# Performance work log

Measured on AMD Instinct MI355X. Metric: run time of the kernel, lower is better.

The kernel has to match this reference:

```python
import jax, jax.numpy as jnp
import numpy as np

NUM_BLOCKS = 8
D_MODEL = 256
FLAT_DIM = NUM_BLOCKS * NUM_BLOCKS + NUM_BLOCKS * 4  # 96


def setup_inputs() -> dict:
    key = jax.random.key(0)
    k1, k2, k3, k4, k5 = jax.random.split(key, 5)
    B, S, Blk = 8, 16384, NUM_BLOCKS
    bit_tensor = jax.random.randint(k1, (B, S, Blk, 8), 0, 2, dtype=jnp.int32)
    macro_stimulus = jax.random.uniform(k2, (B, S), dtype=jnp.float32)
    # torch.rand(...) * 0.1 equivalent (diag masking done in reference, as in torch)
    W_init = jax.random.uniform(k3, (B, S, Blk, Blk), dtype=jnp.float32) * 0.1
    lin_w = jax.random.normal(k4, (D_MODEL, FLAT_DIM), dtype=jnp.float32) / np.sqrt(FLAT_DIM)
    lin_b = jax.random.normal(k5, (D_MODEL,), dtype=jnp.float32) * 0.01
    return {
        "bit_tensor": bit_tensor,
        "macro_stimulus": macro_stimulus,
        "W_init": W_init,
        "lin_w": lin_w,
        "lin_b": lin_b,
        "internal_steps": 10,
    }


def _decode_bits_to_epgl(bit_tensor):
    # [B,S,Blk,8] int bits -> [B,S,Blk,4] floats in {0, 1/3, 2/3, 1}
    b = bit_tensor.astype(jnp.float32)
    return (b[..., 0::2] * 2.0 + b[..., 1::2]) / 3.0  # pairs (0,1),(2,3),(4,5),(6,7) -> E,P,G,L


def _safe_pdist(h):
    # pairwise L2 over last dim: h [B,S,Blk,4] -> [B,S,Blk,Blk]; sqrt-safe at 0 (diagonal)
    diff = h[..., :, None, :] - h[..., None, :, :]
    d2 = jnp.sum(diff * diff, axis=-1)
    return jnp.where(d2 > 0, jnp.sqrt(jnp.where(d2 > 0, d2, 1.0)), 0.0)


def _step(h, W, stim, eye):
    clamp = lambda x: jnp.clip(x, 0.0, 1.0)
    E, P, G, L = h[..., 0], h[..., 1], h[..., 2], h[..., 3]
    W_ns = W * (1.0 - eye)
    inflow = jnp.matmul(W_ns, h)                         # [B,S,Blk,4]
    total_w = jnp.sum(W_ns, axis=-1, keepdims=True) + 1e-8
    neigh = inflow / total_w
    En, Pn, Gn, Ln = neigh[..., 0], neigh[..., 1], neigh[..., 2], neigh[..., 3]
    E_new = clamp(E + 0.3 * stim - 0.4 * P - 0.2 * G)
    P_new = clamp(P + 0.5 * stim + 0.3 * (Pn - P) - 0.2 * E)
    G_new = clamp(G + 0.4 * E * (1.0 - P) + 0.2 * (Gn - G) - 0.3 * P)
    good_neighbor = 0.5 * En + 0.5 * Gn
    L_new = clamp(L + 0.4 * good_neighbor + 0.3 * (Ln - L) - 0.3 * P)
    h_new = jnp.stack([E_new, P_new, G_new, L_new], axis=-1)
    h_diff = _safe_pdist(h_new)                          # cdist(h_new, h_new, p=2)
    mutual_L = (L_new[..., :, None] + L_new[..., None, :]) * 0.5
    W_new = clamp(W + 0.1 * mutual_L * h_diff - 0.05 * W) * (1.0 - eye)
    return h_new, W_new


def _forward(bit_tensor, macro_stimulus, W_init, lin_w, lin_b, internal_steps):
    B, S, Blk, _ = bit_tensor.shape
    eye = jnp.eye(Blk, dtype=jnp.float32)
    h = _decode_bits_to_epgl(bit_tensor)                 # [B,S,Blk,4]
    W = W_init * (1.0 - eye)                             # [B,S,Blk,Blk]
    stim = jnp.broadcast_to(macro_stimulus[..., None], (B, S, Blk))

    def body(carry, _):
        h, W = carry
        h, W = _step(h, W, stim, eye)
        return (h, W), None

    (h, W), _ = jax.lax.scan(body, (h, W), None, length=internal_steps)
    phys = jnp.concatenate([h.reshape(B, S, -1), W.reshape(B, S, -1)], axis=-1)  # [B,S,96]
    macro_embedding = jnp.einsum('bsf,df->bsd', phys, lin_w) + lin_b
    return macro_embedding, h, W


def reference(bit_tensor, macro_stimulus, W_init, lin_w, lin_b, internal_steps):
    return _forward(bit_tensor, macro_stimulus, W_init, lin_w, lin_b, internal_steps)
```

## Files before the change

### kernel.cpp

```cpp
#include <hip/hip_runtime.h>

#define NB 8
#define DM 256
#define FD 96
#define SLD 104

using half8 = _Float16 __attribute__((ext_vector_type(8)));
using half4 = _Float16 __attribute__((ext_vector_type(4)));
using f32x4 = float __attribute__((ext_vector_type(4)));
using f2    = float __attribute__((ext_vector_type(2)));

__device__ __forceinline__ float clamp01(float x) { return fminf(fmaxf(x, 0.0f), 1.0f); }

__global__ void bprep_kernel(const float* __restrict__ lin_w,
                             _Float16* __restrict__ Bpre)
{
    const int fb = blockIdx.x * 256 + threadIdx.x;
    const int ks = fb >> 10, nbv = (fb >> 6) & 15, ll = fb & 63;
    const float* lwrow = lin_w + (size_t)(nbv * 16 + (ll & 15)) * FD
                               + (ks * 32 + 4 * (ll >> 4));
    float4 lo = *reinterpret_cast<const float4*>(lwrow);
    float4 hi = *reinterpret_cast<const float4*>(lwrow + 16);
    half8 v;
    v[0] = (_Float16)lo.x; v[1] = (_Float16)lo.y; v[2] = (_Float16)lo.z; v[3] = (_Float16)lo.w;
    v[4] = (_Float16)hi.x; v[5] = (_Float16)hi.y; v[6] = (_Float16)hi.z; v[7] = (_Float16)hi.w;
    *reinterpret_cast<half8*>(Bpre + (size_t)fb * 8) = v;
}

__global__ __launch_bounds__(256, 2) void fused_kernel(
    const int* __restrict__ bits,
    const float* __restrict__ stim_in,
    const float* __restrict__ Winit,
    const int* __restrict__ steps_ptr,
    const _Float16* __restrict__ Bpre,
    const float* __restrict__ lin_b,
    float* __restrict__ out_emb,
    float* __restrict__ out_h,
    float* __restrict__ out_W)
{
    __shared__ __align__(16) char smem[64 * 132 * 4];
    _Float16* S    = reinterpret_cast<_Float16*>(smem);
    float*    Cbuf = reinterpret_cast<float*>(smem);

    const int tid  = threadIdx.x;
    const int pos0 = blockIdx.x * 128;
    const int p    = tid >> 1;
    const int pos  = pos0 + p;
    const int sub  = tid & 1;
    const int steps = steps_ptr[0];

    f2 hA[8];
    f2 hB[8];
    f2 W2[4][4];

    const int4* bp = reinterpret_cast<const int4*>(bits + (size_t)pos * 64 + sub * 32);
    #pragma unroll
    for (int b = 0; b < 4; ++b) {
        int4 lo = bp[2 * b + 0];
        int4 hi = bp[2 * b + 1];
        hA[b].x = (float)(lo.x * 2 + lo.y) / 3.0f;
        hA[b].y = (float)(lo.z * 2 + lo.w) / 3.0f;
        hB[b].x = (float)(hi.x * 2 + hi.y) / 3.0f;
        hB[b].y = (float)(hi.z * 2 + hi.w) / 3.0f;
    }
    #pragma unroll
    for (int b = 0; b < 4; ++b) {
        hA[4 + b].x = __shfl_xor(hA[b].x, 1, 64);
        hA[4 + b].y = __shfl_xor(hA[b].y, 1, 64);
        hB[4 + b].x = __shfl_xor(hB[b].x, 1, 64);
        hB[4 + b].y = __shfl_xor(hB[b].y, 1, 64);
    }

    const int co_own = sub * 4;
    const int co_oth = 4 - sub * 4;
    #pragma unroll
    for (int i = 0; i < 4; ++i) {
        const float* rowp = Winit + (size_t)pos * 64 + (size_t)(co_own + i) * 8;
        float4 a = *reinterpret_cast<const float4*>(rowp + co_own);
        float4 b = *reinterpret_cast<const float4*>(rowp + co_oth);
        W2[i][0] = (f2){a.x, a.y};
        W2[i][1] = (f2){a.z, a.w};
        W2[i][2] = (f2){b.x, b.y};
        W2[i][3] = (f2){b.z, b.w};
        if (i & 1) W2[i][i >> 1].y = 0.0f; else W2[i][i >> 1].x = 0.0f;
    }

    const float stim = stim_in[pos];

    for (int st = 0; st < steps; ++st) {
        f2 nbA[4], nbB[4];
        #pragma unroll
        for (int i = 0; i < 4; ++i) {
            f2 sA = {0.f, 0.f}, sB = {0.f, 0.f};
            #pragma unroll
            for (int jc = 0; jc < 4; ++jc) {
                f2 wv = W2[i][jc];
                f2 w0 = {wv.x, wv.x};
                f2 w1 = {wv.y, wv.y};
                sA = __builtin_elementwise_fma(w0, hA[2 * jc],     sA);
                sA = __builtin_elementwise_fma(w1, hA[2 * jc + 1], sA);
                sB = __builtin_elementwise_fma(w0, hB[2 * jc],     sB);
                sB = __builtin_elementwise_fma(w1, hB[2 * jc + 1], sB);
            }
            float tw = W2[i][0].x; tw += W2[i][0].y;
            tw += W2[i][1].x;      tw += W2[i][1].y;
            tw += W2[i][2].x;      tw += W2[i][2].y;
            tw += W2[i][3].x;      tw += W2[i][3].y;
            float inv = __builtin_amdgcn_rcpf(tw + 1e-8f);
            f2 inv2 = {inv, inv};
            nbA[i] = sA * inv2;
            nbB[i] = sB * inv2;
        }
        #pragma unroll
        for (int i = 0; i < 4; ++i) {
            float E = hA[i].x, P = hA[i].y, G = hB[i].x, L = hB[i].y;
            float En = nbA[i].x, Pn = nbA[i].y, Gn = nbB[i].x, Ln = nbB[i].y;
            float E_new = clamp01(E + 0.3f * stim - 0.4f * P - 0.2f * G);
            float P_new = clamp01(P + 0.5f * stim + 0.3f * (Pn - P) - 0.2f * E);
            float G_new = clamp01(G + 0.4f * E * (1.0f - P) + 0.2f * (Gn - G) - 0.3f * P);
            float good  = 0.5f * En + 0.5f * Gn;
            float L_new = clamp01(L + 0.4f * good + 0.3f * (Ln - L) - 0.3f * P);
            hA[i] = (f2){E_new, P_new};
            hB[i] = (f2){G_new, L_new};
        }
        #pragma unroll
        for (int b = 0; b < 4; ++b) {
            hA[4 + b].x = __shfl_xor(hA[b].x, 1, 64);
            hA[4 + b].y = __shfl_xor(hA[b].y, 1, 64);
            hB[4 + b].x = __shfl_xor(hB[b].x, 1, 64);
            hB[4 + b].y = __shfl_xor(hB[b].y, 1, 64);
        }
        #pragma unroll
        for (int i = 0; i < 4; ++i) {
            #pragma unroll
            for (int j = i + 1; j < 8; ++j) {
                float d0 = hA[i].x - hA[j].x;
                float d1 = hA[i].y - hA[j].y;
                float d2 = hB[i].x - hB[j].x;
                float d3 = hB[i].y - hB[j].y;
                float q = d0 * d0 + d1 * d1 + d2 * d2 + d3 * d3;
                float dist = __builtin_amdgcn_sqrtf(q);
                float inc = 0.1f * (0.5f * (hB[i].y + hB[j].y)) * dist;
                float wij = (j & 1) ? W2[i][j >> 1].y : W2[i][j >> 1].x;
                wij = clamp01(wij + inc - 0.05f * wij);
                if (j & 1) W2[i][j >> 1].y = wij; else W2[i][j >> 1].x = wij;
                if (j < 4) {
                    float wji = (i & 1) ? W2[j][i >> 1].y : W2[j][i >> 1].x;
                    wji = clamp01(wji + inc - 0.05f * wji);
                    if (i & 1) W2[j][i >> 1].y = wji; else W2[j][i >> 1].x = wji;
                }
            }
        }
    }

    {
        _Float16* sp = S + p * SLD;
        half8 v0, v1;
        v0[0] = (_Float16)hA[0].x; v0[1] = (_Float16)hA[0].y;
        v0[2] = (_Float16)hB[0].x; v0[3] = (_Float16)hB[0].y;
        v0[4] = (_Float16)hA[1].x; v0[5] = (_Float16)hA[1].y;
        v0[6] = (_Float16)hB[1].x; v0[7] = (_Float16)hB[1].y;
        v1[0] = (_Float16)hA[2].x; v1[1] = (_Float16)hA[2].y;
        v1[2] = (_Float16)hB[2].x; v1[3] = (_Float16)hB[2].y;
        v1[4] = (_Float16)hA[3].x; v1[5] = (_Float16)hA[3].y;
        v1[6] = (_Float16)hB[3].x; v1[7] = (_Float16)hB[3].y;
        *reinterpret_cast<half8*>(sp + sub * 16)     = v0;
        *reinterpret_cast<half8*>(sp + sub * 16 + 8) = v1;
        #pragma unroll
        for (int i = 0; i < 4; ++i) {
            half8 wv;
            #pragma unroll
            for (int gc = 0; gc < 8; ++gc) {
                const int lc0 = gc;
                const int lc1 = (gc + 4) & 7;
                float vs0 = (lc0 & 1) ? W2[i][lc0 >> 1].y : W2[i][lc0 >> 1].x;
                float vs1 = (lc1 & 1) ? W2[i][lc1 >> 1].y : W2[i][lc1 >> 1].x;
                wv[gc] = (_Float16)((sub == 0) ? vs0 : vs1);
            }
            *reinterpret_cast<half8*>(sp + 32 + (co_own + i) * 8) = wv;
        }
    }
    __syncthreads();

    #pragma unroll
    for (int i = 0; i < 4; ++i) {
        const int flat4 = i * 1024 + tid * 4;
        const int row = flat4 >> 5, feat = flat4 & 31;
        half4 v = *reinterpret_cast<const half4*>(S + row * SLD + feat);
        float4 o = make_float4((float)v[0], (float)v[1], (float)v[2], (float)v[3]);
        *reinterpret_cast<float4*>(out_h + (size_t)pos0 * 32 + flat4) = o;
    }
    #pragma unroll
    for (int i = 0; i < 8; ++i) {
        const int flat4 = i * 1024 + tid * 4;
        const int row = flat4 >> 6, feat = flat4 & 63;
        half4 v = *reinterpret_cast<const half4*>(S + row * SLD + 32 + feat);
        float4 o = make_float4((float)v[0], (float)v[1], (float)v[2], (float)v[3]);
        *reinterpret_cast<float4*>(out_W + (size_t)pos0 * 64 + flat4) = o;
    }

    const int w = tid >> 6, l = tid & 63;
    const int k0q = 4 * (l >> 4);
    half8 afr[2][3];
    #pragma unroll
    for (int t = 0; t < 2; ++t) {
        const int r = t * 64 + w * 16 + (l & 15);
        #pragma unroll
        for (int ks = 0; ks < 3; ++ks) {
            half4 lo = *reinterpret_cast<const half4*>(S + r * SLD + ks * 32 + k0q);
            half4 hi = *reinterpret_cast<const half4*>(S + r * SLD + ks * 32 + 16 + k0q);
            afr[t][ks] = __builtin_shufflevector(lo, hi, 0, 1, 2, 3, 4, 5, 6, 7);
        }
    }
    __syncthreads();

    #pragma unroll
    for (int t = 0; t < 2; ++t) {
        f32x4 acc[16];
        #pragma unroll
        for (int nbv = 0; nbv < 16; ++nbv) acc[nbv] = (f32x4){0.f, 0.f, 0.f, 0.f};
        #pragma unroll
        for (int ks = 0; ks < 3; ++ks) {
            #pragma unroll
            for (int nbv = 0; nbv < 16; ++nbv) {
                half8 b = *reinterpret_cast<const half8*>(Bpre + (size_t)((ks * 16 + nbv) * 64 + l) * 8);
                acc[nbv] = __builtin_amdgcn_mfma_f32_16x16x32_f16(afr[t][ks], b, acc[nbv], 0, 0, 0);
            }
        }
        #pragma unroll
        for (int c = 0; c < 2; ++c) {
            #pragma unroll
            for (int nn = 0; nn < 8; ++nn) {
                const int nbv = c * 8 + nn;
                #pragma unroll
                for (int r = 0; r < 4; ++r) {
                    const int row = w * 16 + 4 * (l >> 4) + r;
                    Cbuf[row * 132 + nn * 16 + (l & 15)] = acc[nbv][r];
                }
            }
            __syncthreads();
            const float4 biasv = reinterpret_cast<const float4*>(lin_b)[c * 32 + (l & 31)];
            #pragma unroll
            for (int rep = 0; rep < 8; ++rep) {
                const int row = w * 16 + rep * 2 + (l >> 5);
                float4 v = *reinterpret_cast<const float4*>(Cbuf + row * 132 + (l & 31) * 4);
                v.x += biasv.x; v.y += biasv.y; v.z += biasv.z; v.w += biasv.w;
                *reinterpret_cast<float4*>(out_emb + (size_t)(pos0 + t * 64 + row) * DM
                                           + c * 128 + (l & 31) * 4) = v;
            }
            __syncthreads();
        }
    }
}

extern "C" void kernel_launch(void* const* d_in, const int* in_sizes, int n_in,
                              void* d_out, int out_size, void* d_ws, size_t ws_size,
                              hipStream_t stream) {
    const int*   bits  = (const int*)d_in[0];
    const float* stim  = (const float*)d_in[1];
    const float* Winit = (const float*)d_in[2];
    const float* lin_w = (const float*)d_in[3];
    const float* lin_b = (const float*)d_in[4];
    const int*   steps = (const int*)d_in[5];

    const int npos = in_sizes[1];

    float* out_emb = (float*)d_out;
    float* out_h   = out_emb + (size_t)npos * DM;
    float* out_W   = out_h + (size_t)npos * 32;
    _Float16* Bpre = (_Float16*)d_ws;

    hipLaunchKernelGGL(bprep_kernel, dim3(12), dim3(256), 0, stream, lin_w, Bpre);
    hipLaunchKernelGGL(fused_kernel, dim3(npos / 128), dim3(256), 0, stream,
                       bits, stim, Winit, steps, Bpre, lin_b,
                       out_emb, out_h, out_W);
}
```

Baseline: 75.25 us.

## Assign one position per thread, drop shuffles, write MFMA output directly

Each thread now owns a whole 8-block position, so the two-thread split and its per-step cross-lane shuffles go away and W is held as a full 8x8 register tile. The symmetric W update is vectorised with packed two-wide math. The epilogue writes MFMA accumulators plus bias straight to global memory instead of staging them through LDS with extra barriers. In exchange register pressure roughly doubles (launch bounds relaxed to one block per SIMD hint), the grid halves to 256 positions per block, and the output stores become narrower and less coalesced.

```diff
diff --git a/kernel.cpp b/kernel.cpp
--- a/kernel.cpp
+++ b/kernel.cpp
@@ -11,6 +11,10 @@
 using f2    = float __attribute__((ext_vector_type(2)));
 
 __device__ __forceinline__ float clamp01(float x) { return fminf(fmaxf(x, 0.0f), 1.0f); }
+__device__ __forceinline__ f2 pkclamp01(f2 x) {
+    const f2 lo = {0.0f, 0.0f}, hi = {1.0f, 1.0f};
+    return __builtin_elementwise_min(__builtin_elementwise_max(x, lo), hi);
+}
 
 __global__ void bprep_kernel(const float* __restrict__ lin_w,
                              _Float16* __restrict__ Bpre)
@@ -27,7 +31,7 @@
     *reinterpret_cast<half8*>(Bpre + (size_t)fb * 8) = v;
 }
 
-__global__ __launch_bounds__(256, 2) void fused_kernel(
+__global__ __launch_bounds__(256, 1) void fused_kernel(
     const int* __restrict__ bits,
     const float* __restrict__ stim_in,
     const float* __restrict__ Winit,
@@ -38,24 +42,20 @@
     float* __restrict__ out_h,
     float* __restrict__ out_W)
 {
-    __shared__ __align__(16) char smem[64 * 132 * 4];
-    _Float16* S    = reinterpret_cast<_Float16*>(smem);
-    float*    Cbuf = reinterpret_cast<float*>(smem);
+    __shared__ __align__(16) _Float16 S[256 * SLD];
 
     const int tid  = threadIdx.x;
-    const int pos0 = blockIdx.x * 128;
-    const int p    = tid >> 1;
-    const int pos  = pos0 + p;
-    const int sub  = tid & 1;
+    const int pos0 = blockIdx.x * 256;
+    const int pos  = pos0 + tid;
     const int steps = steps_ptr[0];
 
     f2 hA[8];
     f2 hB[8];
-    f2 W2[4][4];
-
-    const int4* bp = reinterpret_cast<const int4*>(bits + (size_t)pos * 64 + sub * 32);
-    #pragma unroll
-    for (int b = 0; b < 4; ++b) {
+    f2 W2[8][4];
+
+    const int4* bp = reinterpret_cast<const int4*>(bits + (size_t)pos * 64);
+    #pragma unroll
+    for (int b = 0; b < 8; ++b) {
         int4 lo = bp[2 * b + 0];
         int4 hi = bp[2 * b + 1];
         hA[b].x = (float)(lo.x * 2 + lo.y) / 3.0f;
@@ -63,21 +63,12 @@
         hB[b].x = (float)(hi.x * 2 + hi.y) / 3.0f;
         hB[b].y = (float)(hi.z * 2 + hi.w) / 3.0f;
     }
-    #pragma unroll
-    for (int b = 0; b < 4; ++b) {
-        hA[4 + b].x = __shfl_xor(hA[b].x, 1, 64);
-        hA[4 + b].y = __shfl_xor(hA[b].y, 1, 64);
-        hB[4 + b].x = __shfl_xor(hB[b].x, 1, 64);
-        hB[4 + b].y = __shfl_xor(hB[b].y, 1, 64);
-    }
-
-    const int co_own = sub * 4;
-    const int co_oth = 4 - sub * 4;
-    #pragma unroll
-    for (int i = 0; i < 4; ++i) {
-        const float* rowp = Winit + (size_t)pos * 64 + (size_t)(co_own + i) * 8;
-        float4 a = *reinterpret_cast<const float4*>(rowp + co_own);
-        float4 b = *reinterpret_cast<const float4*>(rowp + co_oth);
+
+    const float4* wp = reinterpret_cast<const float4*>(Winit + (size_t)pos * 64);
+    #pragma unroll
+    for (int i = 0; i < 8; ++i) {
+        float4 a = wp[2 * i + 0];
+        float4 b = wp[2 * i + 1];
         W2[i][0] = (f2){a.x, a.y};
         W2[i][1] = (f2){a.z, a.w};
         W2[i][2] = (f2){b.x, b.y};
@@ -88,9 +79,9 @@
     const float stim = stim_in[pos];
 
     for (int st = 0; st < steps; ++st) {
-        f2 nbA[4], nbB[4];
-        #pragma unroll
-        for (int i = 0; i < 4; ++i) {
+        f2 nbA[8], nbB[8];
+        #pragma unroll
+        for (int i = 0; i < 8; ++i) {
             f2 sA = {0.f, 0.f}, sB = {0.f, 0.f};
             #pragma unroll
             for (int jc = 0; jc < 4; ++jc) {
@@ -112,7 +103,7 @@
             nbB[i] = sB * inv2;
         }
         #pragma unroll
-        for (int i = 0; i < 4; ++i) {
+        for (int i = 0; i < 8; ++i) {
             float E = hA[i].x, P = hA[i].y, G = hB[i].x, L = hB[i].y;
             float En = nbA[i].x, Pn = nbA[i].y, Gn = nbB[i].x, Ln = nbB[i].y;
             float E_new = clamp01(E + 0.3f * stim - 0.4f * P - 0.2f * G);
@@ -124,16 +115,9 @@
             hB[i] = (f2){G_new, L_new};
         }
         #pragma unroll
-        for (int b = 0; b < 4; ++b) {
-            hA[4 + b].x = __shfl_xor(hA[b].x, 1, 64);
-            hA[4 + b].y = __shfl_xor(hA[b].y, 1, 64);
-            hB[4 + b].x = __shfl_xor(hB[b].x, 1, 64);
-            hB[4 + b].y = __shfl_xor(hB[b].y, 1, 64);
-        }
-        #pragma unroll
-        for (int i = 0; i < 4; ++i) {
-            #pragma unroll
-            for (int j = i + 1; j < 8; ++j) {
+        for (int i = 0; i < 8; ++i) {
+            if ((i & 1) == 0) {
+                const int j = i + 1;
                 float d0 = hA[i].x - hA[j].x;
                 float d1 = hA[i].y - hA[j].y;
                 float d2 = hB[i].x - hB[j].x;
@@ -141,49 +125,63 @@
                 float q = d0 * d0 + d1 * d1 + d2 * d2 + d3 * d3;
                 float dist = __builtin_amdgcn_sqrtf(q);
                 float inc = 0.1f * (0.5f * (hB[i].y + hB[j].y)) * dist;
-                float wij = (j & 1) ? W2[i][j >> 1].y : W2[i][j >> 1].x;
-                wij = clamp01(wij + inc - 0.05f * wij);
-                if (j & 1) W2[i][j >> 1].y = wij; else W2[i][j >> 1].x = wij;
-                if (j < 4) {
-                    float wji = (i & 1) ? W2[j][i >> 1].y : W2[j][i >> 1].x;
-                    wji = clamp01(wji + inc - 0.05f * wji);
-                    if (i & 1) W2[j][i >> 1].y = wji; else W2[j][i >> 1].x = wji;
-                }
+                float wij = W2[i][i >> 1].y;
+                float wji = W2[j][i >> 1].x;
+                W2[i][i >> 1].y = clamp01(wij + inc - 0.05f * wij);
+                W2[j][i >> 1].x = clamp01(wji + inc - 0.05f * wji);
+            }
+            #pragma unroll
+            for (int c = 0; c < 4; ++c) {
+                if (c <= (i >> 1)) continue;
+                const int j1 = 2 * c, j2 = 2 * c + 1;
+                f2 iAx = {hA[i].x, hA[i].x}, iAy = {hA[i].y, hA[i].y};
+                f2 iBx = {hB[i].x, hB[i].x}, iBy = {hB[i].y, hB[i].y};
+                f2 d0v = iAx - (f2){hA[j1].x, hA[j2].x};
+                f2 d1v = iAy - (f2){hA[j1].y, hA[j2].y};
+                f2 d2v = iBx - (f2){hB[j1].x, hB[j2].x};
+                f2 d3v = iBy - (f2){hB[j1].y, hB[j2].y};
+                f2 qv = d0v * d0v + d1v * d1v + d2v * d2v + d3v * d3v;
+                f2 distv = {__builtin_amdgcn_sqrtf(qv.x), __builtin_amdgcn_sqrtf(qv.y)};
+                f2 Lsum  = iBy + (f2){hB[j1].y, hB[j2].y};
+                const f2 c01 = {0.1f, 0.1f}, ch = {0.5f, 0.5f}, c05 = {0.05f, 0.05f};
+                f2 incv = c01 * (ch * Lsum) * distv;
+                f2 Wv = W2[i][c];
+                W2[i][c] = pkclamp01(Wv + incv - c05 * Wv);
+                float wj1 = (i & 1) ? W2[j1][i >> 1].y : W2[j1][i >> 1].x;
+                float wj2 = (i & 1) ? W2[j2][i >> 1].y : W2[j2][i >> 1].x;
+                wj1 = clamp01(wj1 + incv.x - 0.05f * wj1);
+                wj2 = clamp01(wj2 + incv.y - 0.05f * wj2);
+                if (i & 1) { W2[j1][i >> 1].y = wj1; W2[j2][i >> 1].y = wj2; }
+                else       { W2[j1][i >> 1].x = wj1; W2[j2][i >> 1].x = wj2; }
             }
         }
     }
 
     {
-        _Float16* sp = S + p * SLD;
-        half8 v0, v1;
-        v0[0] = (_Float16)hA[0].x; v0[1] = (_Float16)hA[0].y;
-        v0[2] = (_Float16)hB[0].x; v0[3] = (_Float16)hB[0].y;
-        v0[4] = (_Float16)hA[1].x; v0[5] = (_Float16)hA[1].y;
-        v0[6] = (_Float16)hB[1].x; v0[7] = (_Float16)hB[1].y;
-        v1[0] = (_Float16)hA[2].x; v1[1] = (_Float16)hA[2].y;
-        v1[2] = (_Float16)hB[2].x; v1[3] = (_Float16)hB[2].y;
-        v1[4] = (_Float16)hA[3].x; v1[5] = (_Float16)hA[3].y;
-        v1[6] = (_Float16)hB[3].x; v1[7] = (_Float16)hB[3].y;
-        *reinterpret_cast<half8*>(sp + sub * 16)     = v0;
-        *reinterpret_cast<half8*>(sp + sub * 16 + 8) = v1;
-        #pragma unroll
-        for (int i = 0; i < 4; ++i) {
+        _Float16* sp = S + tid * SLD;
+        #pragma unroll
+        for (int b2 = 0; b2 < 4; ++b2) {
+            half8 v;
+            v[0] = (_Float16)hA[2 * b2].x;     v[1] = (_Float16)hA[2 * b2].y;
+            v[2] = (_Float16)hB[2 * b2].x;     v[3] = (_Float16)hB[2 * b2].y;
+            v[4] = (_Float16)hA[2 * b2 + 1].x; v[5] = (_Float16)hA[2 * b2 + 1].y;
+            v[6] = (_Float16)hB[2 * b2 + 1].x; v[7] = (_Float16)hB[2 * b2 + 1].y;
+            *reinterpret_cast<half8*>(sp + b2 * 8) = v;
+        }
+        #pragma unroll
+        for (int r = 0; r < 8; ++r) {
             half8 wv;
-            #pragma unroll
-            for (int gc = 0; gc < 8; ++gc) {
-                const int lc0 = gc;
-                const int lc1 = (gc + 4) & 7;
-                float vs0 = (lc0 & 1) ? W2[i][lc0 >> 1].y : W2[i][lc0 >> 1].x;
-                float vs1 = (lc1 & 1) ? W2[i][lc1 >> 1].y : W2[i][lc1 >> 1].x;
-                wv[gc] = (_Float16)((sub == 0) ? vs0 : vs1);
-            }
-            *reinterpret_cast<half8*>(sp + 32 + (co_own + i) * 8) = wv;
+            wv[0] = (_Float16)W2[r][0].x; wv[1] = (_Float16)W2[r][0].y;
+            wv[2] = (_Float16)W2[r][1].x; wv[3] = (_Float16)W2[r][1].y;
+            wv[4] = (_Float16)W2[r][2].x; wv[5] = (_Float16)W2[r][2].y;
+            wv[6] = (_Float16)W2[r][3].x; wv[7] = (_Float16)W2[r][3].y;
+            *reinterpret_cast<half8*>(sp + 32 + r * 8) = wv;
         }
     }
     __syncthreads();
 
     #pragma unroll
-    for (int i = 0; i < 4; ++i) {
+    for (int i = 0; i < 8; ++i) {
         const int flat4 = i * 1024 + tid * 4;
         const int row = flat4 >> 5, feat = flat4 & 31;
         half4 v = *reinterpret_cast<const half4*>(S + row * SLD + feat);
@@ -191,7 +189,7 @@
         *reinterpret_cast<float4*>(out_h + (size_t)pos0 * 32 + flat4) = o;
     }
     #pragma unroll
-    for (int i = 0; i < 8; ++i) {
+    for (int i = 0; i < 16; ++i) {
         const int flat4 = i * 1024 + tid * 4;
         const int row = flat4 >> 6, feat = flat4 & 63;
         half4 v = *reinterpret_cast<const half4*>(S + row * SLD + 32 + feat);
@@ -201,21 +199,21 @@
 
     const int w = tid >> 6, l = tid & 63;
     const int k0q = 4 * (l >> 4);
-    half8 afr[2][3];
-    #pragma unroll
-    for (int t = 0; t < 2; ++t) {
+    float blin[16];
+    #pragma unroll
+    for (int nbv = 0; nbv < 16; ++nbv)
+        blin[nbv] = lin_b[nbv * 16 + (l & 15)];
+
+    #pragma unroll
+    for (int t = 0; t < 4; ++t) {
         const int r = t * 64 + w * 16 + (l & 15);
+        half8 afr[3];
         #pragma unroll
         for (int ks = 0; ks < 3; ++ks) {
             half4 lo = *reinterpret_cast<const half4*>(S + r * SLD + ks * 32 + k0q);
             half4 hi = *reinterpret_cast<const half4*>(S + r * SLD + ks * 32 + 16 + k0q);
-            afr[t][ks] = __builtin_shufflevector(lo, hi, 0, 1, 2, 3, 4, 5, 6, 7);
-        }
-    }
-    __syncthreads();
-
-    #pragma unroll
-    for (int t = 0; t < 2; ++t) {
+            afr[ks] = __builtin_shufflevector(lo, hi, 0, 1, 2, 3, 4, 5, 6, 7);
+        }
         f32x4 acc[16];
         #pragma unroll
         for (int nbv = 0; nbv < 16; ++nbv) acc[nbv] = (f32x4){0.f, 0.f, 0.f, 0.f};
@@ -224,31 +222,15 @@
             #pragma unroll
             for (int nbv = 0; nbv < 16; ++nbv) {
                 half8 b = *reinterpret_cast<const half8*>(Bpre + (size_t)((ks * 16 + nbv) * 64 + l) * 8);
-                acc[nbv] = __builtin_amdgcn_mfma_f32_16x16x32_f16(afr[t][ks], b, acc[nbv], 0, 0, 0);
-            }
-        }
-        #pragma unroll
-        for (int c = 0; c < 2; ++c) {
-            #pragma unroll
-            for (int nn = 0; nn < 8; ++nn) {
-                const int nbv = c * 8 + nn;
-                #pragma unroll
-                for (int r = 0; r < 4; ++r) {
-                    const int row = w * 16 + 4 * (l >> 4) + r;
-                    Cbuf[row * 132 + nn * 16 + (l & 15)] = acc[nbv][r];
-                }
-            }
-            __syncthreads();
-            const float4 biasv = reinterpret_cast<const float4*>(lin_b)[c * 32 + (l & 31)];
-            #pragma unroll
-            for (int rep = 0; rep < 8; ++rep) {
-                const int row = w * 16 + rep * 2 + (l >> 5);
-                float4 v = *reinterpret_cast<const float4*>(Cbuf + row * 132 + (l & 31) * 4);
-                v.x += biasv.x; v.y += biasv.y; v.z += biasv.z; v.w += biasv.w;
-                *reinterpret_cast<float4*>(out_emb + (size_t)(pos0 + t * 64 + row) * DM
-                                           + c * 128 + (l & 31) * 4) = v;
-            }
-            __syncthreads();
+                acc[nbv] = __builtin_amdgcn_mfma_f32_16x16x32_f16(afr[ks], b, acc[nbv], 0, 0, 0);
+            }
+        }
+        #pragma unroll
+        for (int reg = 0; reg < 4; ++reg) {
+            float* outp = out_emb + (size_t)(pos0 + t * 64 + w * 16 + 4 * (l >> 4) + reg) * DM + (l & 15);
+            #pragma unroll
+            for (int nbv = 0; nbv < 16; ++nbv)
+                outp[nbv * 16] = acc[nbv][reg] + blin[nbv];
         }
     }
 }
@@ -271,7 +253,7 @@
     _Float16* Bpre = (_Float16*)d_ws;
 
     hipLaunchKernelGGL(bprep_kernel, dim3(12), dim3(256), 0, stream, lin_w, Bpre);
-    hipLaunchKernelGGL(fused_kernel, dim3(npos / 128), dim3(256), 0, stream,
+    hipLaunchKernelGGL(fused_kernel, dim3(npos / 256), dim3(256), 0, stream,
                        bits, stim, Winit, steps, Bpre, lin_b,
                        out_emb, out_h, out_W);
 }
```

Result: slower. 81.82 us (+8.7%).
